# Kernel optimization log

Measured on AMD Instinct MI355X. Metric: run time of the kernel, lower is better.

Reference implementation:

```python
import jax, jax.numpy as jnp
import numpy as np

K = 32        # top-k per row (init kwarg k)
TAU = 1.0     # gumbel temperature (init kwarg tau)
EPS = 1e-08
NEG_INF = -1e9


def setup_inputs() -> dict:
    key = jax.random.key(0)
    k1, k2 = jax.random.split(key)
    N = 8192
    logits = jax.random.normal(k1, (N, N), dtype=jnp.float32)
    u = jax.random.uniform(k2, (N, N), dtype=jnp.float32)
    return {"logits": logits, "u": u}


def reference(logits, u):
    # Gumbel noise: -log(-log(U + eps) + eps), matching torch.rand_like usage
    gumbel = -jnp.log(-jnp.log(u + EPS) + EPS)
    perturbed = (logits + gumbel) / TAU
    # Row-wise top-k indices on perturbed logits
    _, top_idx = jax.lax.top_k(perturbed, K)          # [N, K]
    # Scatter a hard 0/1 mask at the selected indices
    N = logits.shape[0]
    rows = jnp.arange(N)[:, None]                      # [N, 1]
    mask = jnp.zeros_like(logits).at[rows, top_idx].set(1.0)
    # Masked softmax over the ORIGINAL logits (noise only selects)
    masked_logits = logits * mask + (1.0 - mask) * NEG_INF
    adjacency = jax.nn.softmax(masked_logits, axis=-1)
    return adjacency
```

## Files before the change

### kernel.cpp

```cpp
#include <hip/hip_runtime.h>
#include <cstdint>

#define ROW_N 8192
#define TPB   256
#define CAP   512

__device__ __forceinline__ unsigned int fkey(float p) {
  unsigned int b = __float_as_uint(p);
  return (b & 0x80000000u) ? ~b : (b | 0x80000000u);
}
__device__ __forceinline__ float fkey_inv(unsigned int t) {
  unsigned int b = (t & 0x80000000u) ? (t & 0x7fffffffu) : ~t;
  return __uint_as_float(b);
}

__device__ __forceinline__ unsigned int akey(float lg, float uu) {
  float l2u = __log2f(uu + 1e-8f);
  float w   = fmaf(l2u, -0.6931471805599453f, 1e-8f);
  float p2  = fmaf(lg, 1.4426950408889634f, -__log2f(w));
  p2 = (w < 1e-5f) ? 3.0e38f : p2;
  return fkey(p2);
}

__device__ __forceinline__ uint64_t shfl_xor_u64(uint64_t v, int m) {
  unsigned int lo = (unsigned int)v, hi = (unsigned int)(v >> 32);
  lo = __shfl_xor(lo, m, 64);
  hi = __shfl_xor(hi, m, 64);
  return ((uint64_t)hi << 32) | lo;
}
__device__ __forceinline__ uint64_t wave_max_u64(uint64_t v) {
#pragma unroll
  for (int s = 32; s >= 1; s >>= 1) {
    uint64_t o = shfl_xor_u64(v, s);
    v = (o > v) ? o : v;
  }
  return v;
}

__global__ __launch_bounds__(TPB) void gumbel_topk_kernel(
    const float* __restrict__ logits, const float* __restrict__ u,
    float* __restrict__ out) {
  const int row  = blockIdx.x;
  const int tid  = threadIdx.x;
  const int lane = tid & 63;
  const int wave = tid >> 6;

  __shared__ unsigned int s_cnt, s_t;
  __shared__ unsigned int s_tmax[TPB];
  __shared__ unsigned int s_idx[CAP];
  __shared__ uint64_t     s_comp[CAP];
  __shared__ float        s_lg[CAP];
  __shared__ float        s_red[8];

  if (tid == 0) { s_cnt = 0; s_t = 0xFFFFFFFFu; }

  const float4* L4 = reinterpret_cast<const float4*>(logits) + (size_t)row * (ROW_N / 4);
  const float4* U4 = reinterpret_cast<const float4*>(u)      + (size_t)row * (ROW_N / 4);
  float4*       O4 = reinterpret_cast<float4*>(out)          + (size_t)row * (ROW_N / 4);

  unsigned int k[32];
  unsigned int M = 0;
#pragma unroll
  for (int j = 0; j < 8; ++j) {
    float4 lv = L4[j * TPB + tid];
    float4 uv = U4[j * TPB + tid];
    k[j * 4 + 0] = akey(lv.x, uv.x);
    k[j * 4 + 1] = akey(lv.y, uv.y);
    k[j * 4 + 2] = akey(lv.z, uv.z);
    k[j * 4 + 3] = akey(lv.w, uv.w);
    M = max(M, max(max(k[j * 4 + 0], k[j * 4 + 1]), max(k[j * 4 + 2], k[j * 4 + 3])));
  }

  {
    float4 z = make_float4(0.f, 0.f, 0.f, 0.f);
#pragma unroll
    for (int j = 0; j < 8; ++j) O4[j * TPB + tid] = z;
  }

  s_tmax[tid] = M;
  __syncthreads();
  {
    unsigned int cnt = 0;
    const uint4* tm4 = reinterpret_cast<const uint4*>(s_tmax);
#pragma unroll 4
    for (int i = 0; i < TPB / 4; ++i) {
      uint4 v = tm4[i];
      cnt += (v.x > M) + (v.y > M) + (v.z > M) + (v.w > M);
    }
    if (cnt < 32) atomicMin(&s_t, M);
  }
  __syncthreads();
  const unsigned int tm = fkey(fkey_inv(s_t) - 0.25f);

#pragma unroll
  for (int j = 0; j < 8; ++j) {
#pragma unroll
    for (int c = 0; c < 4; ++c) {
      if (k[j * 4 + c] >= tm) {
        unsigned int slot = atomicAdd(&s_cnt, 1u);
        if (slot < CAP)
          s_idx[slot] = (unsigned int)(j * TPB + tid) * 4u + (unsigned int)c;
      }
    }
  }
  __syncthreads();
  unsigned int C = s_cnt;

  if (C > CAP) {
#pragma unroll 1
    for (int it = 0; it < 32; ++it) {
      uint64_t lm = 0;
#pragma unroll
      for (int i = 0; i < 32; ++i) {
        unsigned int idx = (unsigned int)((i >> 2) * TPB + tid) * 4u + (unsigned int)(i & 3);
        uint64_t comp = ((uint64_t)k[i] << 13) | (uint64_t)(8191u - idx);
        if (k[i] != 0u && comp > lm) lm = comp;
      }
      uint64_t wm = wave_max_u64(lm);
      if (lm == wm) {
#pragma unroll
        for (int i = 0; i < 32; ++i) {
          unsigned int idx = (unsigned int)((i >> 2) * TPB + tid) * 4u + (unsigned int)(i & 3);
          uint64_t comp = ((uint64_t)k[i] << 13) | (uint64_t)(8191u - idx);
          if (comp == wm) k[i] = 0u;
        }
      }
      if (lane == 0) s_idx[wave * 32 + it] = 8191u - (unsigned int)(wm & 8191u);
    }
    __syncthreads();
    C = 128;
  }

  const float* Lrow = logits + (size_t)row * ROW_N;
  const float* Urow = u      + (size_t)row * ROW_N;
#pragma unroll 1
  for (unsigned int vi = tid; vi < C; vi += TPB) {
    unsigned int idx = s_idx[vi];
    float lg = Lrow[idx];
    float uu = Urow[idx];
    float p  = lg - logf(-logf(uu + 1e-8f) + 1e-8f);
    s_comp[vi] = ((uint64_t)fkey(p) << 13) | (uint64_t)(8191u - idx);
    s_lg[vi]   = lg;
  }
  __syncthreads();

  float m_local = -3.4e38f;
  unsigned int sel = 0;
  float lgs[2];
  unsigned int ids[2];
#pragma unroll
  for (int s = 0; s < 2; ++s) {
    unsigned int vi = tid + s * TPB;
    lgs[s] = 0.f; ids[s] = 0;
    if (vi < C) {
      uint64_t mine = s_comp[vi];
      unsigned int cnt = 0;
#pragma unroll 1
      for (unsigned int i = 0; i < C; ++i) cnt += (s_comp[i] > mine) ? 1u : 0u;
      if (cnt < 32) {
        sel |= (1u << s);
        lgs[s] = s_lg[vi];
        ids[s] = s_idx[vi];
        m_local = fmaxf(m_local, lgs[s]);
      }
    }
  }

  float m = m_local;
#pragma unroll
  for (int s = 32; s >= 1; s >>= 1) m = fmaxf(m, __shfl_xor(m, s, 64));
  if (lane == 0) s_red[wave] = m;
  __syncthreads();
  m = fmaxf(fmaxf(s_red[0], s_red[1]), fmaxf(s_red[2], s_red[3]));

  float e0 = (sel & 1u) ? expf(lgs[0] - m) : 0.f;
  float e1 = (sel & 2u) ? expf(lgs[1] - m) : 0.f;
  float sum = e0 + e1;
#pragma unroll
  for (int s = 32; s >= 1; s >>= 1) sum += __shfl_xor(sum, s, 64);
  if (lane == 0) s_red[4 + wave] = sum;
  __syncthreads();
  sum = (s_red[4] + s_red[5]) + (s_red[6] + s_red[7]);

  float* Orow = out + (size_t)row * ROW_N;
  if (sel & 1u) Orow[ids[0]] = e0 / sum;
  if (sel & 2u) Orow[ids[1]] = e1 / sum;
}

extern "C" void kernel_launch(void* const* d_in, const int* in_sizes, int n_in,
                              void* d_out, int out_size, void* d_ws, size_t ws_size,
                              hipStream_t stream) {
  const float* logits = (const float*)d_in[0];
  const float* u      = (const float*)d_in[1];
  float*       out    = (float*)d_out;
  int rows = in_sizes[0] / ROW_N;
  gumbel_topk_kernel<<<dim3(rows), dim3(TPB), 0, stream>>>(logits, u, out);
}
```

Baseline: 616.9 us.

## Hoist loads, group-reduce threshold search, vectorize rank count, set occupancy bound

Issues all logits/u loads up front and moves zero-fill stores before key computation to increase memory-level parallelism. Replaces the 256-way threshold count with a 4-thread shuffle max followed by a 64-way count, cutting shared-memory work. The candidate rank loop reads two 64-bit keys per LDS access, with a zero sentinel for odd counts. Adds launch_bounds occupancy hint of 4; the coarser threshold may admit more candidates and the load hoisting raises register pressure.

```diff
diff --git a/kernel.cpp b/kernel.cpp
--- a/kernel.cpp
+++ b/kernel.cpp
@@ -37,7 +37,9 @@
   return v;
 }
 
-__global__ __launch_bounds__(TPB) void gumbel_topk_kernel(
+struct alignas(16) u64x2 { uint64_t a, b; };
+
+__global__ __launch_bounds__(TPB, 4) void gumbel_topk_kernel(
     const float* __restrict__ logits, const float* __restrict__ u,
     float* __restrict__ out) {
   const int row  = blockIdx.x;
@@ -46,9 +48,9 @@
   const int wave = tid >> 6;
 
   __shared__ unsigned int s_cnt, s_t;
-  __shared__ unsigned int s_tmax[TPB];
+  __shared__ alignas(16) unsigned int s_gmax[64];
   __shared__ unsigned int s_idx[CAP];
-  __shared__ uint64_t     s_comp[CAP];
+  __shared__ alignas(16) uint64_t s_comp[CAP + 2];
   __shared__ float        s_lg[CAP];
   __shared__ float        s_red[8];
 
@@ -58,36 +60,46 @@
   const float4* U4 = reinterpret_cast<const float4*>(u)      + (size_t)row * (ROW_N / 4);
   float4*       O4 = reinterpret_cast<float4*>(out)          + (size_t)row * (ROW_N / 4);
 
+  float4 lv[8], uv[8];
+#pragma unroll
+  for (int j = 0; j < 8; ++j) {
+    lv[j] = L4[j * TPB + tid];
+    uv[j] = U4[j * TPB + tid];
+  }
+
+  {
+    float4 z = make_float4(0.f, 0.f, 0.f, 0.f);
+#pragma unroll
+    for (int j = 0; j < 8; ++j) O4[j * TPB + tid] = z;
+  }
+
   unsigned int k[32];
   unsigned int M = 0;
 #pragma unroll
   for (int j = 0; j < 8; ++j) {
-    float4 lv = L4[j * TPB + tid];
-    float4 uv = U4[j * TPB + tid];
-    k[j * 4 + 0] = akey(lv.x, uv.x);
-    k[j * 4 + 1] = akey(lv.y, uv.y);
-    k[j * 4 + 2] = akey(lv.z, uv.z);
-    k[j * 4 + 3] = akey(lv.w, uv.w);
+    k[j * 4 + 0] = akey(lv[j].x, uv[j].x);
+    k[j * 4 + 1] = akey(lv[j].y, uv[j].y);
+    k[j * 4 + 2] = akey(lv[j].z, uv[j].z);
+    k[j * 4 + 3] = akey(lv[j].w, uv[j].w);
     M = max(M, max(max(k[j * 4 + 0], k[j * 4 + 1]), max(k[j * 4 + 2], k[j * 4 + 3])));
   }
 
   {
-    float4 z = make_float4(0.f, 0.f, 0.f, 0.f);
-#pragma unroll
-    for (int j = 0; j < 8; ++j) O4[j * TPB + tid] = z;
-  }
-
-  s_tmax[tid] = M;
-  __syncthreads();
-  {
+    unsigned int g = max(M, (unsigned int)__shfl_xor(M, 1, 64));
+    g = max(g, (unsigned int)__shfl_xor(g, 2, 64));
+    if ((tid & 3) == 0) s_gmax[tid >> 2] = g;
+  }
+  __syncthreads();
+  if (tid < 64) {
+    unsigned int mine = s_gmax[tid];
     unsigned int cnt = 0;
-    const uint4* tm4 = reinterpret_cast<const uint4*>(s_tmax);
-#pragma unroll 4
-    for (int i = 0; i < TPB / 4; ++i) {
-      uint4 v = tm4[i];
-      cnt += (v.x > M) + (v.y > M) + (v.z > M) + (v.w > M);
-    }
-    if (cnt < 32) atomicMin(&s_t, M);
+    const uint4* gm4 = reinterpret_cast<const uint4*>(s_gmax);
+#pragma unroll
+    for (int i = 0; i < 16; ++i) {
+      uint4 v = gm4[i];
+      cnt += (v.x > mine) + (v.y > mine) + (v.z > mine) + (v.w > mine);
+    }
+    if (cnt < 32) atomicMin(&s_t, mine);
   }
   __syncthreads();
   const unsigned int tm = fkey(fkey_inv(s_t) - 0.25f);
@@ -142,12 +154,14 @@
     s_comp[vi] = ((uint64_t)fkey(p) << 13) | (uint64_t)(8191u - idx);
     s_lg[vi]   = lg;
   }
+  if (tid == 0) s_comp[C] = 0;
   __syncthreads();
 
   float m_local = -3.4e38f;
   unsigned int sel = 0;
   float lgs[2];
   unsigned int ids[2];
+  const unsigned int CP = (C + 1u) >> 1;
 #pragma unroll
   for (int s = 0; s < 2; ++s) {
     unsigned int vi = tid + s * TPB;
@@ -155,8 +169,13 @@
     if (vi < C) {
       uint64_t mine = s_comp[vi];
       unsigned int cnt = 0;
+      const u64x2* c2 = reinterpret_cast<const u64x2*>(s_comp);
 #pragma unroll 1
-      for (unsigned int i = 0; i < C; ++i) cnt += (s_comp[i] > mine) ? 1u : 0u;
+      for (unsigned int i = 0; i < CP; ++i) {
+        u64x2 v = c2[i];
+        cnt += (v.a > mine) ? 1u : 0u;
+        cnt += (v.b > mine) ? 1u : 0u;
+      }
       if (cnt < 32) {
         sel |= (1u << s);
         lgs[s] = s_lg[vi];
```

Result: faster. 599.6 us (-2.8%).
